# Performance work log

Hardware: AMD Instinct MI355X
Metric: run time of the kernel (lower is better)

## Reference

```python
import jax, jax.numpy as jnp
import numpy as np

B, N, DIM = 1, 65536, 256
H, D, G = 8, 64, 64  # heads, dim_head, slice_num


def setup_inputs() -> dict:
    key = jax.random.key(0)
    ks = jax.random.split(key, 16)
    s = 0.02
    return {
        "x": jax.random.normal(ks[0], (B, N, DIM), jnp.float32),
        "Wx": jax.random.normal(ks[1], (H * D, DIM), jnp.float32) * s,
        "bx": jnp.zeros((H * D,), jnp.float32),
        "Wt1": jax.random.normal(ks[2], (G, D), jnp.float32) * s,
        "bt1": jnp.zeros((G,), jnp.float32),
        "Wt2": jax.random.normal(ks[3], (1, G), jnp.float32) * s,
        "bt2": jnp.zeros((1,), jnp.float32),
        "bias": jnp.ones((1, H, 1, 1), jnp.float32) * 0.5,
        "Ws": jax.random.normal(ks[4], (G, D), jnp.float32) * s,
        "bs": jnp.zeros((G,), jnp.float32),
        "Wq": jax.random.normal(ks[5], (D, D), jnp.float32) * s,
        "Wk": jax.random.normal(ks[6], (D, D), jnp.float32) * s,
        "Wv": jax.random.normal(ks[7], (D, D), jnp.float32) * s,
        "Wout": jax.random.normal(ks[8], (DIM, H * D), jnp.float32) * s,
        "bout": jnp.zeros((DIM,), jnp.float32),
        "u": jax.random.uniform(ks[9], (B, H, N, G), jnp.float32),
    }


def _gelu(t):
    return jax.nn.gelu(t, approximate=False)  # torch default exact GELU


def reference(x, Wx, bx, Wt1, bt1, Wt2, bt2, bias, Ws, bs, Wq, Wk, Wv, Wout, bout, u):
    b, n, _ = x.shape
    h, d, g = Wt1.shape[1] and bias.shape[1], Wq.shape[0], Ws.shape[0]
    # project and split heads: b n (h d) -> b h n d
    x_mid = (x @ Wx.T + bx).reshape(b, n, h, d).transpose(0, 2, 1, 3)
    # per-point temperature MLP + learned bias, clamped
    temp = _gelu(_gelu(x_mid @ Wt1.T + bt1) @ Wt2.T + bt2) + bias  # (b,h,n,1)
    temp = jnp.maximum(temp, 0.01)
    # gumbel-softmax slice routing (soft, hard=False)
    logits = x_mid @ Ws.T + bs  # (b,h,n,g)
    gnoise = -jnp.log(-jnp.log(u + 1e-8) + 1e-8)
    slice_weights = jax.nn.softmax((logits + gnoise) / temp, axis=-1)
    norm = slice_weights.sum(axis=2)  # (b,h,g)
    # gather-aggregate points into g slice tokens
    slice_tokens = jnp.einsum('bhnc,bhng->bhgc', x_mid, slice_weights)
    slice_tokens = slice_tokens / (norm[..., None] + 1e-5)
    # tiny g x g attention among slice tokens
    q = slice_tokens @ Wq.T
    k = slice_tokens @ Wk.T
    v = slice_tokens @ Wv.T
    attn = jax.nn.softmax((q @ k.transpose(0, 1, 3, 2)) * (d ** -0.5), axis=-1)
    out_slice = attn @ v  # (b,h,g,d)
    # scatter-combine back to points
    out = jnp.einsum('bhgd,bhng->bhnd', out_slice, slice_weights)
    out = out.transpose(0, 2, 1, 3).reshape(b, n, h * d)
    return out @ Wout.T + bout
```

## Files before the change

### kernel.cpp

```cpp
#include <hip/hip_runtime.h>
#include <math.h>

#define NPTS  65536
#define DIMX  256
#define NH    8
#define HDIM  512

typedef __attribute__((ext_vector_type(4))) float f32x4;
typedef __attribute__((ext_vector_type(8))) short short8;
typedef __attribute__((ext_vector_type(8))) unsigned short ushort8;
typedef __attribute__((ext_vector_type(4))) unsigned short us4;

__device__ __forceinline__ ushort f2bf(float f) {
    unsigned x = __float_as_uint(f);
    return (ushort)((x + 0x7fffu + ((x >> 16) & 1u)) >> 16);
}
__device__ __forceinline__ float bf2f(ushort u) {
    return __uint_as_float((unsigned)u << 16);
}
__device__ __forceinline__ float erf_fast(float x) {
    float ax = fabsf(x);
    float t  = __builtin_amdgcn_rcpf(1.0f + 0.3275911f * ax);
    float p  = fmaf(fmaf(fmaf(fmaf(1.061405429f, t, -1.453152027f), t,
                   1.421413741f), t, -0.284496736f), t, 0.254829592f) * t;
    float y  = 1.0f - p * __expf(-ax * ax);
    return copysignf(y, x);
}
__device__ __forceinline__ float gelu_fast(float x) {
    return 0.5f * x * (1.0f + erf_fast(x * 0.7071067811865476f));
}

__global__ __launch_bounds__(256)
void gemm_xmid_kernel(const float* __restrict__ A, const float* __restrict__ B,
                      const float* __restrict__ bias, ushort* __restrict__ C) {
    __shared__ __align__(16) ushort Al[128][64];
    __shared__ __align__(16) ushort Bl[128][64];
    const int m0 = blockIdx.x * 128, n0 = blockIdx.y * 128;
    const int t = threadIdx.x, l = t & 63, w = t >> 6;
    const int wr = w >> 1, wc = w & 1;
    const int lr = l & 15, lq = l >> 4;

    f32x4 acc[4][4];
    #pragma unroll
    for (int mi = 0; mi < 4; ++mi)
        #pragma unroll
        for (int ni = 0; ni < 4; ++ni) acc[mi][ni] = (f32x4){0.f, 0.f, 0.f, 0.f};

    for (int ks = 0; ks < 4; ++ks) {
        __syncthreads();
        #pragma unroll
        for (int i = 0; i < 4; ++i) {
            int idx = i * 256 + t;
            int row = idx >> 3, g = idx & 7;
            const float* ap = &A[(size_t)(m0 + row) * 256 + ks * 64 + g * 8];
            float4 a0 = *(const float4*)ap;
            float4 a1 = *(const float4*)(ap + 4);
            ushort8 av = { f2bf(a0.x), f2bf(a0.y), f2bf(a0.z), f2bf(a0.w),
                           f2bf(a1.x), f2bf(a1.y), f2bf(a1.z), f2bf(a1.w) };
            *(ushort8*)&Al[row][(g ^ (row & 7)) * 8] = av;
            const float* bp = &B[(size_t)(n0 + row) * 256 + ks * 64 + g * 8];
            float4 b0 = *(const float4*)bp;
            float4 b1 = *(const float4*)(bp + 4);
            ushort8 bv = { f2bf(b0.x), f2bf(b0.y), f2bf(b0.z), f2bf(b0.w),
                           f2bf(b1.x), f2bf(b1.y), f2bf(b1.z), f2bf(b1.w) };
            *(ushort8*)&Bl[row][(g ^ (row & 7)) * 8] = bv;
        }
        __syncthreads();
        #pragma unroll
        for (int kf = 0; kf < 2; ++kf) {
            short8 af[4], bfr[4];
            #pragma unroll
            for (int mi = 0; mi < 4; ++mi) {
                int row = wr * 64 + mi * 16 + lr, g = kf * 4 + lq;
                af[mi] = *(const short8*)&Al[row][(g ^ (row & 7)) * 8];
            }
            #pragma unroll
            for (int ni = 0; ni < 4; ++ni) {
                int row = wc * 64 + ni * 16 + lr, g = kf * 4 + lq;
                bfr[ni] = *(const short8*)&Bl[row][(g ^ (row & 7)) * 8];
            }
            #pragma unroll
            for (int mi = 0; mi < 4; ++mi)
                #pragma unroll
                for (int ni = 0; ni < 4; ++ni)
                    acc[mi][ni] = __builtin_amdgcn_mfma_f32_16x16x32_bf16(
                        af[mi], bfr[ni], acc[mi][ni], 0, 0, 0);
        }
    }
    #pragma unroll
    for (int ni = 0; ni < 4; ++ni) {
        int col = n0 + wc * 64 + ni * 16 + lr;
        float bb = bias[col];
        #pragma unroll
        for (int mi = 0; mi < 4; ++mi)
            #pragma unroll
            for (int j = 0; j < 4; ++j) {
                int row = m0 + wr * 64 + mi * 16 + lq * 4 + j;
                C[(size_t)row * 512 + col] = f2bf(acc[mi][ni][j] + bb);
            }
    }
}

__global__ __launch_bounds__(256)
void lgt1_mfma_kernel(const ushort* __restrict__ xmb,
                      const float* __restrict__ Ws,  const float* __restrict__ bs,
                      const float* __restrict__ Wt1, const float* __restrict__ bt1,
                      const float* __restrict__ Wt2, const float* __restrict__ bt2,
                      const float* __restrict__ biasp,
                      const float* __restrict__ u,
                      ushort* __restrict__ swb) {
    __shared__ __align__(16) ushort Al[128][64];
    __shared__ __align__(16) ushort Bl[128][64];
    const int h = blockIdx.y, m0 = blockIdx.x * 128;
    const int t = threadIdx.x, l = t & 63, w = t >> 6;
    const int lr = l & 15, lq = l >> 4;

    #pragma unroll
    for (int i = 0; i < 4; ++i) {
        int idx = i * 256 + t;
        int row = idx >> 3, g = idx & 7;
        ushort8 av = *(const ushort8*)&xmb[(size_t)(m0 + row) * 512 + h * 64 + g * 8];
        *(ushort8*)&Al[row][(g ^ (row & 7)) * 8] = av;
        const float* src = (row < 64 ? &Ws[(size_t)row * 64]
                                     : &Wt1[(size_t)(row - 64) * 64]) + g * 8;
        float4 b0 = *(const float4*)src;
        float4 b1 = *(const float4*)(src + 4);
        ushort8 bv = { f2bf(b0.x), f2bf(b0.y), f2bf(b0.z), f2bf(b0.w),
                       f2bf(b1.x), f2bf(b1.y), f2bf(b1.z), f2bf(b1.w) };
        *(ushort8*)&Bl[row][(g ^ (row & 7)) * 8] = bv;
    }
    __syncthreads();

    f32x4 acc[2][8];
    #pragma unroll
    for (int mi = 0; mi < 2; ++mi)
        #pragma unroll
        for (int ni = 0; ni < 8; ++ni) acc[mi][ni] = (f32x4){0.f, 0.f, 0.f, 0.f};

    #pragma unroll
    for (int kf = 0; kf < 2; ++kf) {
        short8 af[2], bfr[8];
        #pragma unroll
        for (int mi = 0; mi < 2; ++mi) {
            int row = w * 32 + mi * 16 + lr, g = kf * 4 + lq;
            af[mi] = *(const short8*)&Al[row][(g ^ (row & 7)) * 8];
        }
        #pragma unroll
        for (int ni = 0; ni < 8; ++ni) {
            int row = ni * 16 + lr, g = kf * 4 + lq;
            bfr[ni] = *(const short8*)&Bl[row][(g ^ (row & 7)) * 8];
        }
        #pragma unroll
        for (int mi = 0; mi < 2; ++mi)
            #pragma unroll
            for (int ni = 0; ni < 8; ++ni)
                acc[mi][ni] = __builtin_amdgcn_mfma_f32_16x16x32_bf16(
                    af[mi], bfr[ni], acc[mi][ni], 0, 0, 0);
    }

    const float bt2v = bt2[0], biasph = biasp[h];
    float bsr[4], bt1r[4], wt2r[4];
    #pragma unroll
    for (int ni = 0; ni < 4; ++ni) {
        bsr[ni]  = bs [ni * 16 + lr];
        bt1r[ni] = bt1[ni * 16 + lr];
        wt2r[ni] = Wt2[ni * 16 + lr];
    }

    #pragma unroll
    for (int mi = 0; mi < 2; ++mi)
        #pragma unroll
        for (int jj = 0; jj < 4; ++jj) {
            const int n = m0 + w * 32 + mi * 16 + lq * 4 + jj;
            float tsum = 0.f;
            #pragma unroll
            for (int ni = 0; ni < 4; ++ni)
                tsum += gelu_fast(acc[mi][ni + 4][jj] + bt1r[ni]) * wt2r[ni];
            tsum += __shfl_xor(tsum, 1);
            tsum += __shfl_xor(tsum, 2);
            tsum += __shfl_xor(tsum, 4);
            tsum += __shfl_xor(tsum, 8);
            float temp = gelu_fast(tsum + bt2v) + biasph;
            temp = fmaxf(temp, 0.01f);
            const float invt = __builtin_amdgcn_rcpf(temp);

            const float* up = &u[((size_t)h * NPTS + n) * 64 + lr];
            float s[4];
            float ps = 0.f;
            #pragma unroll
            for (int ni = 0; ni < 4; ++ni) {
                float uu = up[ni * 16];
                float gn = -__logf(-__logf(uu + 1e-8f) + 1e-8f);
                s[ni] = __expf(fmaf(acc[mi][ni][jj] + bsr[ni] + gn, invt, -25.0f));
                ps += s[ni];
            }
            ps += __shfl_xor(ps, 1);
            ps += __shfl_xor(ps, 2);
            ps += __shfl_xor(ps, 4);
            ps += __shfl_xor(ps, 8);
            const float inv = __builtin_amdgcn_rcpf(ps);
            ushort* sp = &swb[(size_t)n * 512 + h * 64 + lr];
            #pragma unroll
            for (int ni = 0; ni < 4; ++ni)
                sp[ni * 16] = f2bf(s[ni] * inv);
        }
}

__global__ __launch_bounds__(256)
void gather_mfma_kernel(const ushort* __restrict__ xmb, const ushort* __restrict__ swb,
                        float* __restrict__ stp, float* __restrict__ normp) {
    __shared__ __align__(16) ushort swT[64][128];
    __shared__ __align__(16) ushort xT [64][128];
    const int h  = blockIdx.y;
    const int n0 = blockIdx.x * 1024;
    const int t  = threadIdx.x, l = t & 63, w = t >> 6;
    const int lr = l & 15, lq = l >> 4;
    const int gb = t & 7;
    const int ng = t >> 3;

    f32x4 acc[4][4];
    #pragma unroll
    for (int gi = 0; gi < 4; ++gi)
        #pragma unroll
        for (int ci = 0; ci < 4; ++ci) acc[gi][ci] = (f32x4){0.f, 0.f, 0.f, 0.f};
    float nrm8[8];
    #pragma unroll
    for (int j = 0; j < 8; ++j) nrm8[j] = 0.f;

    for (int r = 0; r < 8; ++r) {
        const int nt = n0 + r * 128;
        ushort8 sv[4], xv[4];
        #pragma unroll
        for (int i = 0; i < 4; ++i) {
            int n = nt + ng * 4 + i;
            sv[i] = *(const ushort8*)&swb[(size_t)n * 512 + h * 64 + gb * 8];
            xv[i] = *(const ushort8*)&xmb[(size_t)n * 512 + h * 64 + gb * 8];
        }
        __syncthreads();
        #pragma unroll
        for (int j = 0; j < 8; ++j) {
            int g   = gb * 8 + j;
            int swz = (ng >> 1) ^ (g & 7) ^ ((g >> 3) & 7);
            int off = swz * 8 + (ng & 1) * 4;
            us4 s4 = { sv[0][j], sv[1][j], sv[2][j], sv[3][j] };
            us4 x4 = { xv[0][j], xv[1][j], xv[2][j], xv[3][j] };
            *(us4*)&swT[g][off] = s4;
            *(us4*)&xT [g][off] = x4;
            nrm8[j] += (bf2f(sv[0][j]) + bf2f(sv[1][j]))
                     + (bf2f(sv[2][j]) + bf2f(sv[3][j]));
        }
        __syncthreads();
        short8 af[4], bfr[4];
        #pragma unroll
        for (int gi = 0; gi < 4; ++gi) {
            int g   = gi * 16 + lr;
            int swz = (w * 4 + lq) ^ (g & 7) ^ ((g >> 3) & 7);
            af[gi]  = *(const short8*)&swT[g][swz * 8];
            bfr[gi] = *(const short8*)&xT [g][swz * 8];
        }
        #pragma unroll
        for (int gi = 0; gi < 4; ++gi)
            #pragma unroll
            for (int ci = 0; ci < 4; ++ci)
                acc[gi][ci] = __builtin_amdgcn_mfma_f32_16x16x32_bf16(
                    af[gi], bfr[ci], acc[gi][ci], 0, 0, 0);
    }

    const size_t base = ((size_t)h * 256 + blockIdx.x * 4 + w) * 4096;
    #pragma unroll
    for (int gi = 0; gi < 4; ++gi)
        #pragma unroll
        for (int ci = 0; ci < 4; ++ci)
            #pragma unroll
            for (int j = 0; j < 4; ++j)
                stp[base + (size_t)(gi * 16 + lq * 4 + j) * 64 + ci * 16 + lr]
                    = acc[gi][ci][j];

    __syncthreads();
    float* narr = (float*)swT;
    #pragma unroll
    for (int j = 0; j < 8; ++j) narr[ng * 64 + gb * 8 + j] = nrm8[j];
    __syncthreads();
    if (t < 64) {
        float s = 0.f;
        #pragma unroll 8
        for (int k = 0; k < 32; ++k) s += narr[k * 64 + t];
        normp[((size_t)h * 64 + blockIdx.x) * 64 + t] = s;
    }
}

__global__ __launch_bounds__(256)
void reduce_st_kernel(const float* __restrict__ stp, const float* __restrict__ normp,
                      float* __restrict__ st_red, float* __restrict__ nrm) {
    const int h = blockIdx.x;
    const int e = blockIdx.y * 256 + threadIdx.x;
    float s = 0.f;
    #pragma unroll 8
    for (int ch = 0; ch < 256; ++ch)
        s += stp[((size_t)h * 256 + ch) * 4096 + e];
    st_red[(size_t)h * 4096 + e] = s;
    if (blockIdx.y == 0 && threadIdx.x < 64) {
        float ns = 0.f;
        #pragma unroll 8
        for (int ch = 0; ch < 64; ++ch)
            ns += normp[((size_t)h * 64 + ch) * 64 + threadIdx.x];
        nrm[h * 64 + threadIdx.x] = ns + 1e-5f;
    }
}

__global__ __launch_bounds__(256)
void attn_small_kernel(const float* __restrict__ st_red, const float* __restrict__ nrm,
                       const float* __restrict__ Wq, const float* __restrict__ Wk,
                       const float* __restrict__ Wv, float* __restrict__ osl) {
    __shared__ float st[64][68];
    __shared__ float ql[64][68];
    __shared__ float kl[64][68];
    __shared__ float vl[64][68];
    __shared__ float sc[64][68];
    __shared__ float nl[64];
    const int h = blockIdx.x;
    const int t = threadIdx.x;

    if (t < 64) nl[t] = nrm[h * 64 + t];
    __syncthreads();
    for (int e = t; e < 4096; e += 256)
        st[e>>6][e&63] = st_red[(size_t)h * 4096 + e] / nl[e>>6];
    __syncthreads();
    for (int e = t; e < 4096; e += 256) {
        int g = e >> 6, dd = e & 63;
        float aq = 0.f, ak = 0.f, av = 0.f;
        for (int cc = 0; cc < 64; ++cc) {
            float sv = st[g][cc];
            aq = fmaf(sv, Wq[dd*64 + cc], aq);
            ak = fmaf(sv, Wk[dd*64 + cc], ak);
            av = fmaf(sv, Wv[dd*64 + cc], av);
        }
        ql[g][dd] = aq; kl[g][dd] = ak; vl[g][dd] = av;
    }
    __syncthreads();
    for (int e = t; e < 4096; e += 256) {
        int g = e >> 6, gp = e & 63;
        float s = 0.f;
        for (int dd = 0; dd < 64; ++dd) s = fmaf(ql[g][dd], kl[gp][dd], s);
        sc[g][gp] = s * 0.125f;
    }
    __syncthreads();
    if (t < 64) {
        float m = -1e30f;
        for (int j = 0; j < 64; ++j) m = fmaxf(m, sc[t][j]);
        float ssum = 0.f;
        for (int j = 0; j < 64; ++j) { float p = expf(sc[t][j] - m); sc[t][j] = p; ssum += p; }
        float inv = 1.f / ssum;
        for (int j = 0; j < 64; ++j) sc[t][j] *= inv;
    }
    __syncthreads();
    for (int e = t; e < 4096; e += 256) {
        int g = e >> 6, dd = e & 63;
        float s = 0.f;
        for (int gp = 0; gp < 64; ++gp) s = fmaf(sc[g][gp], vl[gp][dd], s);
        osl[(size_t)h * 4096 + e] = s;
    }
}

__global__ __launch_bounds__(256)
void fold_kernel(const float* __restrict__ osl, const float* __restrict__ Wout,
                 float* __restrict__ Mt) {
    __shared__ float os[64][65];
    __shared__ float wl[128][65];
    const int h  = blockIdx.x;
    const int i0 = blockIdx.y * 128;
    const int t  = threadIdx.x;
    for (int e = t; e < 4096; e += 256) os[e>>6][e&63] = osl[(size_t)h * 4096 + e];
    for (int e = t; e < 8192; e += 256) {
        int i = e >> 6, d = e & 63;
        wl[i][d] = Wout[(size_t)(i0 + i) * HDIM + h * 64 + d];
    }
    __syncthreads();
    const int g = t & 63, iq = t >> 6;
    #pragma unroll 4
    for (int k = 0; k < 32; ++k) {
        int i = iq * 32 + k;
        float s = 0.f;
        #pragma unroll
        for (int d = 0; d < 64; ++d) s = fmaf(os[g][d], wl[i][d], s);
        Mt[(size_t)(i0 + i) * HDIM + h * 64 + g] = s;
    }
}

__global__ __launch_bounds__(256)
void gemm_out_kernel(const ushort* __restrict__ A, const float* __restrict__ B,
                     const float* __restrict__ bias, float* __restrict__ C) {
    __shared__ __align__(16) ushort Al[128][64];
    __shared__ __align__(16) ushort Bl[128][64];
    const int m0 = blockIdx.x * 128, n0 = blockIdx.y * 128;
    const int t = threadIdx.x, l = t & 63, w = t >> 6;
    const int wr = w >> 1, wc = w & 1;
    const int lr = l & 15, lq = l >> 4;

    f32x4 acc[4][4];
    #pragma unroll
    for (int mi = 0; mi < 4; ++mi)
        #pragma unroll
        for (int ni = 0; ni < 4; ++ni) acc[mi][ni] = (f32x4){0.f, 0.f, 0.f, 0.f};

    for (int ks = 0; ks < 8; ++ks) {
        __syncthreads();
        #pragma unroll
        for (int i = 0; i < 4; ++i) {
            int idx = i * 256 + t;
            int row = idx >> 3, g = idx & 7;
            ushort8 av = *(const ushort8*)&A[(size_t)(m0 + row) * 512 + ks * 64 + g * 8];
            *(ushort8*)&Al[row][(g ^ (row & 7)) * 8] = av;
            const float* bp = &B[(size_t)(n0 + row) * 512 + ks * 64 + g * 8];
            float4 b0 = *(const float4*)bp;
            float4 b1 = *(const float4*)(bp + 4);
            ushort8 bv = { f2bf(b0.x), f2bf(b0.y), f2bf(b0.z), f2bf(b0.w),
                           f2bf(b1.x), f2bf(b1.y), f2bf(b1.z), f2bf(b1.w) };
            *(ushort8*)&Bl[row][(g ^ (row & 7)) * 8] = bv;
        }
        __syncthreads();
        #pragma unroll
        for (int kf = 0; kf < 2; ++kf) {
            short8 af[4], bfr[4];
            #pragma unroll
            for (int mi = 0; mi < 4; ++mi) {
                int row = wr * 64 + mi * 16 + lr, g = kf * 4 + lq;
                af[mi] = *(const short8*)&Al[row][(g ^ (row & 7)) * 8];
            }
            #pragma unroll
            for (int ni = 0; ni < 4; ++ni) {
                int row = wc * 64 + ni * 16 + lr, g = kf * 4 + lq;
                bfr[ni] = *(const short8*)&Bl[row][(g ^ (row & 7)) * 8];
            }
            #pragma unroll
            for (int mi = 0; mi < 4; ++mi)
                #pragma unroll
                for (int ni = 0; ni < 4; ++ni)
                    acc[mi][ni] = __builtin_amdgcn_mfma_f32_16x16x32_bf16(
                        af[mi], bfr[ni], acc[mi][ni], 0, 0, 0);
        }
    }
    #pragma unroll
    for (int ni = 0; ni < 4; ++ni) {
        int col = n0 + wc * 64 + ni * 16 + lr;
        float bb = bias[col];
        #pragma unroll
        for (int mi = 0; mi < 4; ++mi)
            #pragma unroll
            for (int j = 0; j < 4; ++j) {
                int row = m0 + wr * 64 + mi * 16 + lq * 4 + j;
                C[(size_t)row * 256 + col] = acc[mi][ni][j] + bb;
            }
    }
}

extern "C" void kernel_launch(void* const* d_in, const int* in_sizes, int n_in,
                              void* d_out, int out_size, void* d_ws, size_t ws_size,
                              hipStream_t stream) {
    const float* x    = (const float*)d_in[0];
    const float* Wx   = (const float*)d_in[1];
    const float* bx   = (const float*)d_in[2];
    const float* Wt1  = (const float*)d_in[3];
    const float* bt1  = (const float*)d_in[4];
    const float* Wt2  = (const float*)d_in[5];
    const float* bt2  = (const float*)d_in[6];
    const float* biasp= (const float*)d_in[7];
    const float* Ws   = (const float*)d_in[8];
    const float* bs   = (const float*)d_in[9];
    const float* Wq   = (const float*)d_in[10];
    const float* Wk   = (const float*)d_in[11];
    const float* Wv   = (const float*)d_in[12];
    const float* Wout = (const float*)d_in[13];
    const float* bout = (const float*)d_in[14];
    const float* u    = (const float*)d_in[15];
    float* out = (float*)d_out;

    float*  stp    = (float*)d_ws;
    float*  normp  = stp    + (size_t)NH * 256 * 4096;
    float*  Mt     = normp  + (size_t)NH * 64 * 64;
    float*  st_red = Mt     + (size_t)DIMX * HDIM;
    float*  nrm    = st_red + (size_t)NH * 4096;
    float*  osl    = nrm    + (size_t)NH * 64;
    ushort* xmb    = (ushort*)(osl + (size_t)NH * 4096);
    ushort* swb    = xmb + (size_t)NPTS * HDIM;

    gemm_xmid_kernel<<<dim3(512, 4), 256, 0, stream>>>(x, Wx, bx, xmb);
    lgt1_mfma_kernel<<<dim3(512, 8), 256, 0, stream>>>(xmb, Ws, bs, Wt1, bt1,
                                                       Wt2, bt2, biasp, u, swb);
    gather_mfma_kernel<<<dim3(64, 8), 256, 0, stream>>>(xmb, swb, stp, normp);
    reduce_st_kernel<<<dim3(8, 16), 256, 0, stream>>>(stp, normp, st_red, nrm);
    attn_small_kernel<<<8, 256, 0, stream>>>(st_red, nrm, Wq, Wk, Wv, osl);
    fold_kernel<<<dim3(8, 2), 256, 0, stream>>>(osl, Wout, Mt);
    gemm_out_kernel<<<dim3(512, 2), 256, 0, stream>>>(swb, Mt, bout, out);
}
```

Baseline: 291.1 us.

## Pre-convert routing weights to bf16, prefetch noise, batch softmax reductions in lgt1 kernel

Adds a one-block prep kernel that converts Ws and Wt1 to a bf16 buffer once, so the lgt1 kernel reads B fragments straight from global/L2 and drops its B shared-memory tile and per-block conversion. The gumbel noise tensor u is now loaded early, before the MFMA loop for the first half and after it for the second, to overlap its latency with compute. The temperature and softmax sums are computed for four rows at once with batched shuffles, and log/exp switch to log2/exp2 forms with folded constants. The trade-offs are more live registers, uncoalesced global B-fragment loads in place of LDS reads, and one extra kernel launch.

```diff
diff --git a/kernel.cpp b/kernel.cpp
--- a/kernel.cpp
+++ b/kernel.cpp
@@ -28,6 +28,19 @@
 }
 __device__ __forceinline__ float gelu_fast(float x) {
     return 0.5f * x * (1.0f + erf_fast(x * 0.7071067811865476f));
+}
+
+__global__ __launch_bounds__(256)
+void prep_wb_kernel(const float* __restrict__ Ws, const float* __restrict__ Wt1,
+                    ushort* __restrict__ wb) {
+    const int t = threadIdx.x;
+    #pragma unroll
+    for (int i = 0; i < 32; ++i) {
+        int idx = i * 256 + t;
+        int row = idx >> 6, col = idx & 63;
+        float v = (row < 64) ? Ws[row * 64 + col] : Wt1[(row - 64) * 64 + col];
+        wb[idx] = f2bf(v);
+    }
 }
 
 __global__ __launch_bounds__(256)
@@ -103,17 +116,19 @@
 
 __global__ __launch_bounds__(256)
 void lgt1_mfma_kernel(const ushort* __restrict__ xmb,
-                      const float* __restrict__ Ws,  const float* __restrict__ bs,
-                      const float* __restrict__ Wt1, const float* __restrict__ bt1,
+                      const ushort* __restrict__ wb,
+                      const float* __restrict__ bs,  const float* __restrict__ bt1,
                       const float* __restrict__ Wt2, const float* __restrict__ bt2,
                       const float* __restrict__ biasp,
                       const float* __restrict__ u,
                       ushort* __restrict__ swb) {
     __shared__ __align__(16) ushort Al[128][64];
-    __shared__ __align__(16) ushort Bl[128][64];
     const int h = blockIdx.y, m0 = blockIdx.x * 128;
     const int t = threadIdx.x, l = t & 63, w = t >> 6;
     const int lr = l & 15, lq = l >> 4;
+    const float LOG2E = 1.4426950408889634f;
+    const float LN2   = 0.6931471805599453f;
+    const float SH2   = 36.0673760222f;
 
     #pragma unroll
     for (int i = 0; i < 4; ++i) {
@@ -121,13 +136,15 @@
         int row = idx >> 3, g = idx & 7;
         ushort8 av = *(const ushort8*)&xmb[(size_t)(m0 + row) * 512 + h * 64 + g * 8];
         *(ushort8*)&Al[row][(g ^ (row & 7)) * 8] = av;
-        const float* src = (row < 64 ? &Ws[(size_t)row * 64]
-                                     : &Wt1[(size_t)(row - 64) * 64]) + g * 8;
-        float4 b0 = *(const float4*)src;
-        float4 b1 = *(const float4*)(src + 4);
-        ushort8 bv = { f2bf(b0.x), f2bf(b0.y), f2bf(b0.z), f2bf(b0.w),
-                       f2bf(b1.x), f2bf(b1.y), f2bf(b1.z), f2bf(b1.w) };
-        *(ushort8*)&Bl[row][(g ^ (row & 7)) * 8] = bv;
+    }
+
+    float uu0[4][4];
+    #pragma unroll
+    for (int jj = 0; jj < 4; ++jj) {
+        const int n = m0 + w * 32 + lq * 4 + jj;
+        const float* up = &u[((size_t)h * NPTS + n) * 64 + lr];
+        #pragma unroll
+        for (int ni = 0; ni < 4; ++ni) uu0[jj][ni] = up[ni * 16];
     }
     __syncthreads();
 
@@ -139,23 +156,31 @@
 
     #pragma unroll
     for (int kf = 0; kf < 2; ++kf) {
+        const int g = kf * 4 + lq;
         short8 af[2], bfr[8];
         #pragma unroll
         for (int mi = 0; mi < 2; ++mi) {
-            int row = w * 32 + mi * 16 + lr, g = kf * 4 + lq;
+            int row = w * 32 + mi * 16 + lr;
             af[mi] = *(const short8*)&Al[row][(g ^ (row & 7)) * 8];
         }
         #pragma unroll
-        for (int ni = 0; ni < 8; ++ni) {
-            int row = ni * 16 + lr, g = kf * 4 + lq;
-            bfr[ni] = *(const short8*)&Bl[row][(g ^ (row & 7)) * 8];
-        }
+        for (int ni = 0; ni < 8; ++ni)
+            bfr[ni] = *(const short8*)&wb[(size_t)(ni * 16 + lr) * 64 + g * 8];
         #pragma unroll
         for (int mi = 0; mi < 2; ++mi)
             #pragma unroll
             for (int ni = 0; ni < 8; ++ni)
                 acc[mi][ni] = __builtin_amdgcn_mfma_f32_16x16x32_bf16(
                     af[mi], bfr[ni], acc[mi][ni], 0, 0, 0);
+    }
+
+    float uu1[4][4];
+    #pragma unroll
+    for (int jj = 0; jj < 4; ++jj) {
+        const int n = m0 + w * 32 + 16 + lq * 4 + jj;
+        const float* up = &u[((size_t)h * NPTS + n) * 64 + lr];
+        #pragma unroll
+        for (int ni = 0; ni < 4; ++ni) uu1[jj][ni] = up[ni * 16];
     }
 
     const float bt2v = bt2[0], biasph = biasp[h];
@@ -168,42 +193,58 @@
     }
 
     #pragma unroll
-    for (int mi = 0; mi < 2; ++mi)
+    for (int mi = 0; mi < 2; ++mi) {
+        float ts[4];
+        #pragma unroll
+        for (int jj = 0; jj < 4; ++jj) {
+            float s = 0.f;
+            #pragma unroll
+            for (int ni = 0; ni < 4; ++ni)
+                s += gelu_fast(acc[mi][ni + 4][jj] + bt1r[ni]) * wt2r[ni];
+            ts[jj] = s;
+        }
+        #pragma unroll
+        for (int off = 1; off <= 8; off <<= 1) {
+            #pragma unroll
+            for (int jj = 0; jj < 4; ++jj) ts[jj] += __shfl_xor(ts[jj], off);
+        }
+        float invt[4], invt2[4];
+        #pragma unroll
+        for (int jj = 0; jj < 4; ++jj) {
+            float tmp = gelu_fast(ts[jj] + bt2v) + biasph;
+            tmp = fmaxf(tmp, 0.01f);
+            invt[jj]  = __builtin_amdgcn_rcpf(tmp);
+            invt2[jj] = invt[jj] * LOG2E;
+        }
+        float sv[4][4], ps[4] = {0.f, 0.f, 0.f, 0.f};
+        #pragma unroll
+        for (int jj = 0; jj < 4; ++jj) {
+            #pragma unroll
+            for (int ni = 0; ni < 4; ++ni) {
+                float uuv = (mi == 0 ? uu0[jj][ni] : uu1[jj][ni]);
+                float L1 = __log2f(uuv + 1e-8f);
+                float inner = fmaf(-LN2, L1, 1e-8f);
+                float L2v = __log2f(inner);
+                float base = fmaf(acc[mi][ni][jj] + bsr[ni], invt2[jj], -SH2);
+                sv[jj][ni] = __builtin_amdgcn_exp2f(fmaf(-invt[jj], L2v, base));
+                ps[jj] += sv[jj][ni];
+            }
+        }
+        #pragma unroll
+        for (int off = 1; off <= 8; off <<= 1) {
+            #pragma unroll
+            for (int jj = 0; jj < 4; ++jj) ps[jj] += __shfl_xor(ps[jj], off);
+        }
         #pragma unroll
         for (int jj = 0; jj < 4; ++jj) {
             const int n = m0 + w * 32 + mi * 16 + lq * 4 + jj;
-            float tsum = 0.f;
+            const float inv = __builtin_amdgcn_rcpf(ps[jj]);
+            ushort* sp = &swb[(size_t)n * 512 + h * 64 + lr];
             #pragma unroll
             for (int ni = 0; ni < 4; ++ni)
-                tsum += gelu_fast(acc[mi][ni + 4][jj] + bt1r[ni]) * wt2r[ni];
-            tsum += __shfl_xor(tsum, 1);
-            tsum += __shfl_xor(tsum, 2);
-            tsum += __shfl_xor(tsum, 4);
-            tsum += __shfl_xor(tsum, 8);
-            float temp = gelu_fast(tsum + bt2v) + biasph;
-            temp = fmaxf(temp, 0.01f);
-            const float invt = __builtin_amdgcn_rcpf(temp);
-
-            const float* up = &u[((size_t)h * NPTS + n) * 64 + lr];
-            float s[4];
-            float ps = 0.f;
-            #pragma unroll
-            for (int ni = 0; ni < 4; ++ni) {
-                float uu = up[ni * 16];
-                float gn = -__logf(-__logf(uu + 1e-8f) + 1e-8f);
-                s[ni] = __expf(fmaf(acc[mi][ni][jj] + bsr[ni] + gn, invt, -25.0f));
-                ps += s[ni];
-            }
-            ps += __shfl_xor(ps, 1);
-            ps += __shfl_xor(ps, 2);
-            ps += __shfl_xor(ps, 4);
-            ps += __shfl_xor(ps, 8);
-            const float inv = __builtin_amdgcn_rcpf(ps);
-            ushort* sp = &swb[(size_t)n * 512 + h * 64 + lr];
-            #pragma unroll
-            for (int ni = 0; ni < 4; ++ni)
-                sp[ni * 16] = f2bf(s[ni] * inv);
-        }
+                sp[ni * 16] = f2bf(sv[jj][ni] * inv);
+        }
+    }
 }
 
 __global__ __launch_bounds__(256)
@@ -481,11 +522,13 @@
     float*  st_red = Mt     + (size_t)DIMX * HDIM;
     float*  nrm    = st_red + (size_t)NH * 4096;
     float*  osl    = nrm    + (size_t)NH * 64;
-    ushort* xmb    = (ushort*)(osl + (size_t)NH * 4096);
+    ushort* wb     = (ushort*)(osl + (size_t)NH * 4096);
+    ushort* xmb    = wb  + (size_t)128 * 64;
     ushort* swb    = xmb + (size_t)NPTS * HDIM;
 
+    prep_wb_kernel<<<1, 256, 0, stream>>>(Ws, Wt1, wb);
     gemm_xmid_kernel<<<dim3(512, 4), 256, 0, stream>>>(x, Wx, bx, xmb);
-    lgt1_mfma_kernel<<<dim3(512, 8), 256, 0, stream>>>(xmb, Ws, bs, Wt1, bt1,
+    lgt1_mfma_kernel<<<dim3(512, 8), 256, 0, stream>>>(xmb, wb, bs, bt1,
                                                        Wt2, bt2, biasp, u, swb);
     gather_mfma_kernel<<<dim3(64, 8), 256, 0, stream>>>(xmb, swb, stp, normp);
     reduce_st_kernel<<<dim3(8, 16), 256, 0, stream>>>(stp, normp, st_red, nrm);
```

New measurement: 290.4 us. No clear change (-0.2%).
